# Kernel optimization log

Hardware: AMD Instinct MI355X
Metric: run time of the kernel (lower is better)

## Reference

```python
import jax, jax.numpy as jnp
import numpy as np
import math

EPS = 1e-5
H = 8  # n_heads


def _layernorm(x, g, b):
    mu = jnp.mean(x, axis=-1, keepdims=True)
    var = jnp.var(x, axis=-1, keepdims=True)
    return (x - mu) * jax.lax.rsqrt(var + EPS) * g + b


def _conv1d(x_bdn, w_oik):
    # x: [B, D, N], w: [O, I, K] (torch Conv1d layout), padding = K//2
    k = w_oik.shape[-1]
    p = k // 2
    return jax.lax.conv_general_dilated(
        x_bdn, w_oik, window_strides=(1,), padding=((p, p),),
        dimension_numbers=('NCH', 'OIH', 'NCH'))


def setup_inputs() -> dict:
    key = jax.random.key(0)
    ks = jax.random.split(key, 10)
    B, N, D, dq = 4096, 25, 256, 64
    s = 0.02
    inp = {
        'x': jax.random.normal(ks[0], (B, N, D), jnp.float32),
        'wq': jax.random.normal(ks[1], (D, D, 3), jnp.float32) * s,
        'wk': jax.random.normal(ks[2], (D, D, 3), jnp.float32) * s,
        'wv': jax.random.normal(ks[3], (D, D, 3), jnp.float32) * s,
        'ln_q_g': jnp.ones((D,), jnp.float32), 'ln_q_b': jnp.zeros((D,), jnp.float32),
        'ln_k_g': jnp.ones((D,), jnp.float32), 'ln_k_b': jnp.zeros((D,), jnp.float32),
        'ln_v_g': jnp.ones((D,), jnp.float32), 'ln_v_b': jnp.zeros((D,), jnp.float32),
        'rel_table': jax.random.normal(ks[4], (2 * N - 1, H), jnp.float32) * s,
        'global_bias': jax.random.normal(ks[5], (H, N, N), jnp.float32) * s,
        'alpha': jnp.float32(1.0),
        'wqf': jax.random.normal(ks[6], (D, dq), jnp.float32) * s,
        'bqf': jnp.zeros((dq,), jnp.float32),
        'wqp': jax.random.normal(ks[7], (dq, H), jnp.float32) * s,
        'bqp': jnp.zeros((H,), jnp.float32),
        'wo': jax.random.normal(ks[8], (D, D), jnp.float32) * s,
        'bo': jnp.zeros((D,), jnp.float32),
    }
    return inp


def reference(x, wq, wk, wv, ln_q_g, ln_q_b, ln_k_g, ln_k_b, ln_v_g, ln_v_b,
              rel_table, global_bias, alpha, wqf, bqf, wqp, bqp, wo, bo):
    B, N, D = x.shape
    dk = D // H
    xp = jnp.transpose(x, (0, 2, 1))  # [B, D, N]

    # conv projections + LayerNorm + residual
    q = x + _layernorm(jnp.transpose(_conv1d(xp, wq), (0, 2, 1)), ln_q_g, ln_q_b)
    k = x + _layernorm(jnp.transpose(_conv1d(xp, wk), (0, 2, 1)), ln_k_g, ln_k_b)
    v = x + _layernorm(jnp.transpose(_conv1d(xp, wv), (0, 2, 1)), ln_v_g, ln_v_b)

    q4 = q.reshape(B, N, H, dk)
    k4 = k.reshape(B, N, H, dk)
    v4 = v.reshape(B, N, H, dk)

    scores = jnp.einsum('bnhd,bmhd->bhnm', q4, k4) / math.sqrt(dk)

    # relative position bias: table[(i - j) + N - 1] -> [H, N, N]
    ids = jnp.arange(N)
    rel_idx = ids[:, None] - ids[None, :] + N - 1  # [N, N]
    rel_bias = jnp.transpose(rel_table[rel_idx], (2, 0, 1))  # [H, N, N]
    scores = scores + rel_bias[None] + global_bias[None] * alpha

    # dynamic adjacency bias from pairwise node feature differences
    qf = x @ wqf + bqf  # [B, N, dq]
    pair = jnp.tanh(qf[:, :, None, :] - qf[:, None, :, :])  # [B, N, N, dq]
    dyn = pair @ wqp + bqp  # [B, N, N, H]
    scores = scores + jnp.transpose(dyn, (0, 3, 1, 2))

    attn = jax.nn.softmax(scores, axis=-1)  # [B, H, N, N]
    out = jnp.einsum('bhnm,bmhd->bnhd', attn, v4).reshape(B, N, D)
    return out @ wo + bo
```

## Files before the change

### kernel.cpp

```cpp
#include <hip/hip_runtime.h>
#include <hip/hip_bf16.h>
#include <stdint.h>

using u16 = unsigned short;
using u32 = unsigned int;

typedef __attribute__((ext_vector_type(8))) __bf16 bf16x8;
typedef __attribute__((ext_vector_type(4))) float f32x4;

__device__ __forceinline__ float bf2f(u16 h) {
  u32 u = ((u32)h) << 16;
  return __builtin_bit_cast(float, u);
}
__device__ __forceinline__ u16 f2bf(float f) {
  u32 u = __builtin_bit_cast(u32, f);
  u += 0x7fffu + ((u >> 16) & 1u);
  return (u16)(u >> 16);
}
__device__ __forceinline__ float blo(u32 u) { return __builtin_bit_cast(float, u << 16); }
__device__ __forceinline__ float bhi(u32 u) { return __builtin_bit_cast(float, u & 0xffff0000u); }

__device__ __forceinline__ uint4 cvt8(const float* s) {
  float4 f0 = *(const float4*)s;
  float4 f1 = *(const float4*)(s + 4);
  uint4 r;
  r.x = (u32)f2bf(f0.x) | ((u32)f2bf(f0.y) << 16);
  r.y = (u32)f2bf(f0.z) | ((u32)f2bf(f0.w) << 16);
  r.z = (u32)f2bf(f1.x) | ((u32)f2bf(f1.y) << 16);
  r.w = (u32)f2bf(f1.z) | ((u32)f2bf(f1.w) << 16);
  return r;
}

__device__ __forceinline__ u32 tanh2(u32 a, u32 b) {
  const float d0 = blo(a) - blo(b);
  const float d1 = bhi(a) - bhi(b);
  const float e0 = __expf(2.f * d0), e1 = __expf(2.f * d1);
  const float t0 = 1.f - 2.f * __builtin_amdgcn_rcpf(e0 + 1.f);
  const float t1 = 1.f - 2.f * __builtin_amdgcn_rcpf(e1 + 1.f);
  return (u32)f2bf(t0) | ((u32)f2bf(t1) << 16);
}

__device__ __forceinline__ void gl_lds(const u16* gsrc, u16* ldsbase) {
  __builtin_amdgcn_global_load_lds(
      (const __attribute__((address_space(1))) u32*)gsrc,
      (__attribute__((address_space(3))) u32*)ldsbase, 16, 0, 0);
}


__global__ __launch_bounds__(256) void prep_kernel(
    const float* __restrict__ wq, const float* __restrict__ wk, const float* __restrict__ wv,
    const float* __restrict__ wo, const float* __restrict__ wqf,
    const float* __restrict__ lnqg, const float* __restrict__ lnqb,
    const float* __restrict__ lnkg, const float* __restrict__ lnkb,
    const float* __restrict__ lnvg, const float* __restrict__ lnvb,
    const float* __restrict__ relt, const float* __restrict__ gbias,
    const float* __restrict__ alphap,
    const float* __restrict__ wqp, const float* __restrict__ bqp,
    const float* __restrict__ bqf, const float* __restrict__ bo,
    u16* __restrict__ wT, u16* __restrict__ woT,
    u16* __restrict__ wqfT, u16* __restrict__ params)
{
  long long j = (long long)blockIdx.x * 256 + threadIdx.x;
  if (j < 589824) {
    int col = (int)(j / 768), k = (int)(j % 768);
    int p = col >> 8, o = col & 255, t = k >> 8, i = k & 255;
    const float* w = (p == 0) ? wq : (p == 1) ? wk : wv;
    wT[j] = f2bf(w[o * 768 + i * 3 + t]);
    return;
  }
  j -= 589824;
  if (j < 65536) {
    int n = (int)(j >> 8), k = (int)(j & 255);
    woT[j] = f2bf(wo[k * 256 + n]);
    return;
  }
  j -= 65536;
  if (j < 16384) {
    int col = (int)(j >> 8), k = (int)(j & 255);
    wqfT[j] = f2bf(wqf[k * 64 + col]);
    return;
  }
  j -= 16384;
  if (j < 8864) {
    int t = (int)j;
    if (t >= 8800) { params[t] = 0; return; }
    if (t >= 7776) {
      int t2 = t - 7776;
      int col = t2 >> 6, k = t2 & 63;
      params[t] = (col < 8) ? f2bf(wqp[k * 8 + col]) : (u16)0;
      return;
    }
    if (t >= 1928 && t < 6928) {
      int idx = t - 1928;
      int h = idx / 625, rem = idx % 625, n = rem / 25, m = rem % 25;
      params[t] = f2bf(gbias[idx] * alphap[0] + relt[(n - m + 24) * 8 + h] + bqp[h]);
      return;
    }
    const float* src; int si;
    if (t < 1536) {
      int a = t >> 8, c = t & 255;
      src = (a == 0) ? lnqg : (a == 1) ? lnqb : (a == 2) ? lnkg
          : (a == 3) ? lnkb : (a == 4) ? lnvg : lnvb;
      si = c;
    } else if (t < 1928) { src = relt;  si = t - 1536; }
    else if (t < 6936)   { src = alphap; si = 0; }
    else if (t < 7448)   { src = wqp;   si = t - 6936; }
    else if (t < 7456)   { src = bqp;   si = t - 7448; }
    else if (t < 7520)   { src = bqf;   si = t - 7456; }
    else                 { src = bo;    si = t - 7520; }
    params[t] = f2bf(src[si]);
  }
}

__global__ __launch_bounds__(256) void xconv_kernel(
    const float* __restrict__ x, u16* __restrict__ xbf)
{
  const long long i = ((long long)blockIdx.x * 256 + threadIdx.x) * 8;
  *(uint4*)&xbf[i] = cvt8(x + i);
}

__global__ __launch_bounds__(256) void convln_kernel(
    const u16* __restrict__ xbf, long long row0,
    const u16* __restrict__ wT,
    u16* __restrict__ C,
    const u16* __restrict__ params,
    const u16* __restrict__ zpad)
{
  __shared__ __align__(16) u16 Asm[64 * 64];
  __shared__ __align__(16) u16 Bsm[256 * 64];
  __shared__ float sG[256];
  __shared__ float sB[256];
  __shared__ float sSum[4][64];
  __shared__ float sSq[4][64];

  const int tid = threadIdx.x;
  const int l = tid & 63, w = tid >> 6;
  const int p = blockIdx.x;
  const int c0 = p * 256;
  const int r0 = blockIdx.y * 64;
  const int lrow = l >> 3, chunk = l & 7;
  const int g8 = (l >> 4) * 8, l15 = l & 15;
  const int rbase = 4 * (l >> 4);
  const int swz = l15 & 7;

  sG[tid] = bf2f(params[p * 512 + tid]);
  sB[tid] = bf2f(params[p * 512 + 256 + tid]);

  f32x4 acc[4][4];
#pragma unroll
  for (int m = 0; m < 4; ++m)
#pragma unroll
    for (int n = 0; n < 4; ++n)
      acc[m][n] = (f32x4){0.f, 0.f, 0.f, 0.f};

  for (int ks = 0; ks < 12; ++ks) {
    const int k0 = ks * 64;
    const int t = k0 >> 8, kc = k0 & 255;
    __syncthreads();
#pragma unroll
    for (int it = 0; it < 2; ++it) {
      const int seg = w * 2 + it;
      const int row_l = seg * 8 + lrow;
      const bool valid = ((unsigned)((r0 + row_l) % 25 + t - 1) < 25u);
      const u16* src = valid
          ? xbf + (size_t)(row0 + r0 + row_l + t - 1) * 256 + kc + ((chunk ^ lrow) << 3)
          : zpad;
      gl_lds(src, &Asm[seg * 512]);
    }
#pragma unroll
    for (int it = 0; it < 8; ++it) {
      const int seg = w * 8 + it;
      const int row_l = seg * 8 + lrow;
      const u16* src = wT + (size_t)(c0 + row_l) * 768 + k0 + ((chunk ^ lrow) << 3);
      gl_lds(src, &Bsm[seg * 512]);
    }
    __syncthreads();

#pragma unroll
    for (int kk = 0; kk < 64; kk += 32) {
      const int c = (kk >> 3) + (l >> 4);
      const int co = ((c ^ swz) << 3);
      bf16x8 av[4], bv[4];
#pragma unroll
      for (int m = 0; m < 4; ++m)
        av[m] = *(const bf16x8*)&Asm[(m * 16 + l15) * 64 + co];
#pragma unroll
      for (int n = 0; n < 4; ++n)
        bv[n] = *(const bf16x8*)&Bsm[(w * 64 + n * 16 + l15) * 64 + co];
#pragma unroll
      for (int m = 0; m < 4; ++m)
#pragma unroll
        for (int n = 0; n < 4; ++n)
          acc[m][n] = __builtin_amdgcn_mfma_f32_16x16x32_bf16(av[m], bv[n], acc[m][n], 0, 0, 0);
    }
  }

#pragma unroll
  for (int m = 0; m < 4; ++m) {
#pragma unroll
    for (int r = 0; r < 4; ++r) {
      float s = 0.f, q = 0.f;
#pragma unroll
      for (int n = 0; n < 4; ++n) { const float v = acc[m][n][r]; s += v; q += v * v; }
#pragma unroll
      for (int mk = 1; mk < 16; mk <<= 1) {
        s += __shfl_xor(s, mk, 64);
        q += __shfl_xor(q, mk, 64);
      }
      if (l15 == 0) {
        const int row = m * 16 + rbase + r;
        sSum[w][row] = s;
        sSq[w][row] = q;
      }
    }
  }
  __syncthreads();

#pragma unroll
  for (int m = 0; m < 4; ++m) {
    float mu4[4], rs4[4];
#pragma unroll
    for (int r = 0; r < 4; ++r) {
      const int row = m * 16 + rbase + r;
      const float tot = sSum[0][row] + sSum[1][row] + sSum[2][row] + sSum[3][row];
      const float tq  = sSq[0][row] + sSq[1][row] + sSq[2][row] + sSq[3][row];
      const float mu = tot * (1.f / 256.f);
      const float var = tq * (1.f / 256.f) - mu * mu;
      mu4[r] = mu;
      rs4[r] = rsqrtf(var + 1e-5f);
    }
#pragma unroll
    for (int n = 0; n < 4; ++n) {
      const int lc = w * 64 + n * 16 + l15;
      const float g = sG[lc], bb = sB[lc];
#pragma unroll
      for (int r = 0; r < 4; ++r) {
        const int row = m * 16 + rbase + r;
        const float xv = bf2f(xbf[(size_t)(row0 + r0 + row) * 256 + lc]);
        const float v = (acc[m][n][r] - mu4[r]) * rs4[r] * g + bb + xv;
        C[(size_t)(r0 + row) * 768 + c0 + lc] = f2bf(v);
      }
    }
  }
}

template<int BN, bool HAS_BIAS, bool F32OUT>
__global__ __launch_bounds__(256) void gemm_kernel(
    const u16* __restrict__ A, int lda, long long row0,
    const u16* __restrict__ BT, int ldb,
    void* __restrict__ Cv, int ldc,
    const u16* __restrict__ bias,
    int ksteps)
{
  constexpr int NB = BN / 32;
  __shared__ __align__(16) u16 Asm[128 * 64];
  __shared__ __align__(16) u16 Bsm[BN * 64];

  const int tid = threadIdx.x;
  const int l = tid & 63;
  const int w = tid >> 6;
  const int c0 = blockIdx.x * BN;
  const int r0 = blockIdx.y * 128;
  const int wr = w >> 1, wc = w & 1;

  f32x4 acc[4][NB];
#pragma unroll
  for (int m = 0; m < 4; ++m)
#pragma unroll
    for (int n = 0; n < NB; ++n)
      acc[m][n] = (f32x4){0.f, 0.f, 0.f, 0.f};

  const int lrow = l >> 3;
  const int chunk = l & 7;
  const int l15 = l & 15;
  const int swz = l15 & 7;

  for (int ks = 0; ks < ksteps; ++ks) {
    const int k0 = ks * 64;
    __syncthreads();
#pragma unroll
    for (int it = 0; it < 4; ++it) {
      const int seg = w * 4 + it;
      const int row_l = seg * 8 + lrow;
      const u16* src = A + (size_t)(row0 + r0 + row_l) * lda + k0 + ((chunk ^ lrow) << 3);
      gl_lds(src, &Asm[seg * 512]);
    }
#pragma unroll
    for (int it = 0; it < NB; ++it) {
      const int seg = w * NB + it;
      const int row_l = seg * 8 + lrow;
      const u16* src = BT + (size_t)(c0 + row_l) * ldb + k0 + ((chunk ^ lrow) << 3);
      gl_lds(src, &Bsm[seg * 512]);
    }
    __syncthreads();

#pragma unroll
    for (int kk = 0; kk < 64; kk += 32) {
      const int c = (kk >> 3) + (l >> 4);
      const int co = ((c ^ swz) << 3);
      bf16x8 av[4], bv[NB];
#pragma unroll
      for (int m = 0; m < 4; ++m)
        av[m] = *(const bf16x8*)&Asm[(wr * 64 + m * 16 + l15) * 64 + co];
#pragma unroll
      for (int n = 0; n < NB; ++n)
        bv[n] = *(const bf16x8*)&Bsm[(wc * (BN / 2) + n * 16 + l15) * 64 + co];
#pragma unroll
      for (int m = 0; m < 4; ++m)
#pragma unroll
        for (int n = 0; n < NB; ++n)
          acc[m][n] = __builtin_amdgcn_mfma_f32_16x16x32_bf16(av[m], bv[n], acc[m][n], 0, 0, 0);
    }
  }

  const int rbase = 4 * (l >> 4);
#pragma unroll
  for (int m = 0; m < 4; ++m) {
#pragma unroll
    for (int n = 0; n < NB; ++n) {
      const int col = c0 + wc * (BN / 2) + n * 16 + l15;
      float badd = 0.f;
      if (HAS_BIAS) badd = bf2f(bias[col]);
#pragma unroll
      for (int r = 0; r < 4; ++r) {
        const int row = r0 + wr * 64 + m * 16 + rbase + r;
        const float v = acc[m][n][r] + badd;
        if constexpr (F32OUT) ((float*)Cv)[(size_t)row * ldc + col] = v;
        else                  ((u16*)Cv)[(size_t)row * ldc + col] = f2bf(v);
      }
    }
  }
}

__global__ __launch_bounds__(256) void attn_kernel(
    u16* __restrict__ qkv,
    const u16* __restrict__ qf,
    const u16* __restrict__ params)
{
  __shared__ __align__(16) char arena[38848];
  float* sS    = (float*)arena;
  u16*   sV    = (u16*)(arena + 20000);
  u16*   sQF   = (u16*)(arena + 33200);
  u16*   sWQPT = (u16*)(arena + 36800);

  const int b = blockIdx.x;
  const int tid = threadIdx.x;
  const int w = tid >> 6, l = tid & 63;
  const int g8 = (l >> 4) * 8;
  const int rbase = 4 * (l >> 4);
  const int l15 = l & 15;

  {
    for (int i = tid; i < 800; i += 256) {
      const int m = i >> 5, c8 = (i & 31) * 8;
      *(uint4*)&sV[m * 264 + c8] =
          *(const uint4*)(qkv + (size_t)(b * 25 + m) * 768 + 512 + c8);
    }
    for (int i = tid; i < 200; i += 256) {
      const int r = i >> 3, c8 = (i & 7) * 8;
      *(uint4*)&sQF[r * 72 + c8] = *(const uint4*)(qf + (size_t)b * 1600 + r * 64 + c8);
    }
    for (int i = tid; i < 128; i += 256)
      ((uint4*)sWQPT)[i] = ((const uint4*)(params + 7776))[i];
  }
  __syncthreads();

  f32x4 dt[10];
  {
    const bf16x8 bv0 = *(const bf16x8*)&sWQPT[l15 * 64 + g8];
    const bf16x8 bv1 = *(const bf16x8*)&sWQPT[l15 * 64 + 32 + g8];
#pragma unroll
    for (int ti = 0; ti < 10; ++ti) {
      const int p0 = (ti * 4 + w) * 16;
      int p = p0 + l15; if (p > 624) p = 624;
      const int n = p / 25, m = p % 25;
      const uint4 qn0 = *(const uint4*)&sQF[n * 72 + g8];
      const uint4 qn1 = *(const uint4*)&sQF[n * 72 + 32 + g8];
      const uint4 qm0 = *(const uint4*)&sQF[m * 72 + g8];
      const uint4 qm1 = *(const uint4*)&sQF[m * 72 + 32 + g8];
      u32 a0[4], a1[4];
      a0[0] = tanh2(qn0.x, qm0.x); a0[1] = tanh2(qn0.y, qm0.y);
      a0[2] = tanh2(qn0.z, qm0.z); a0[3] = tanh2(qn0.w, qm0.w);
      a1[0] = tanh2(qn1.x, qm1.x); a1[1] = tanh2(qn1.y, qm1.y);
      a1[2] = tanh2(qn1.z, qm1.z); a1[3] = tanh2(qn1.w, qm1.w);
      const bf16x8 av0 = __builtin_bit_cast(bf16x8, *(uint4*)a0);
      const bf16x8 av1 = __builtin_bit_cast(bf16x8, *(uint4*)a1);
      f32x4 d = (f32x4){0.f, 0.f, 0.f, 0.f};
      d = __builtin_amdgcn_mfma_f32_16x16x32_bf16(av0, bv0, d, 0, 0, 0);
      d = __builtin_amdgcn_mfma_f32_16x16x32_bf16(av1, bv1, d, 0, 0, 0);
      dt[ti] = d;
    }
    bf16x8 zf8;
#pragma unroll
    for (int j = 0; j < 8; ++j) zf8[j] = (__bf16)0.f;
#pragma unroll
    for (int hh = 0; hh < 2; ++hh) {
      const int h = 2 * w + hh;
      bf16x8 qa[2], kb[2];
#pragma unroll
      for (int t = 0; t < 2; ++t) {
        const int row = l15 + 16 * t;
        if (row < 25) {
          const u16* base = qkv + (size_t)(b * 25 + row) * 768 + h * 32 + g8;
          qa[t] = *(const bf16x8*)base;
          kb[t] = *(const bf16x8*)(base + 256);
        } else { qa[t] = zf8; kb[t] = zf8; }
      }
#pragma unroll
      for (int tn = 0; tn < 2; ++tn)
#pragma unroll
        for (int tm = 0; tm < 2; ++tm) {
          f32x4 d = __builtin_amdgcn_mfma_f32_16x16x32_bf16(
              qa[tn], kb[tm], (f32x4){0.f, 0.f, 0.f, 0.f}, 0, 0, 0);
          const int m = l15 + 16 * tm;
#pragma unroll
          for (int r = 0; r < 4; ++r) {
            const int n = rbase + r + 16 * tn;
            if (n < 25 && m < 25) {
              const int idx = h * 625 + n * 25 + m;
              sS[idx] = d[r] * 0.17677669529663687f + bf2f(params[1928 + idx]);
            }
          }
        }
    }
  }
  __syncthreads();

  {
    if (l15 < 8) {
      const int h = l15;
#pragma unroll
      for (int ti = 0; ti < 10; ++ti) {
        const int p0 = (ti * 4 + w) * 16;
#pragma unroll
        for (int r = 0; r < 4; ++r) {
          const int p = p0 + rbase + r;
          if (p < 625) sS[h * 625 + p] += dt[ti][r];
        }
      }
    }
  }
  __syncthreads();

  {
    for (int u = tid; u < 200; u += 256) {
      const int h = u / 25, n = u % 25;
      float* rp = &sS[h * 625 + n * 25];
      float mx = -1e30f;
#pragma unroll
      for (int m = 0; m < 25; ++m) mx = fmaxf(mx, rp[m]);
      float ssum = 0.f;
#pragma unroll
      for (int m = 0; m < 25; ++m) { rp[m] = __expf(rp[m] - mx); ssum += rp[m]; }
      const float inv = __builtin_amdgcn_rcpf(ssum);
#pragma unroll
      for (int m = 0; m < 25; ++m) rp[m] *= inv;
    }
  }
  __syncthreads();

  {
#pragma unroll
    for (int hh = 0; hh < 2; ++hh) {
      const int h = 2 * w + hh;
      bf16x8 pa[2], vb[2];
#pragma unroll
      for (int t = 0; t < 2; ++t) {
        const int n = l15 + 16 * t;
#pragma unroll
        for (int j = 0; j < 8; ++j) {
          const int m = g8 + j;
          const float pv = (n < 25 && m < 25) ? sS[h * 625 + n * 25 + m] : 0.f;
          pa[t][j] = (__bf16)pv;
        }
      }
#pragma unroll
      for (int t = 0; t < 2; ++t) {
        const int dcol = l15 + 16 * t;
#pragma unroll
        for (int j = 0; j < 8; ++j) {
          const int m = g8 + j;
          vb[t][j] = (m < 25)
              ? __builtin_bit_cast(__bf16, sV[m * 264 + h * 32 + dcol])
              : (__bf16)0.f;
        }
      }
#pragma unroll
      for (int tn = 0; tn < 2; ++tn)
#pragma unroll
        for (int td = 0; td < 2; ++td) {
          f32x4 d = __builtin_amdgcn_mfma_f32_16x16x32_bf16(
              pa[tn], vb[td], (f32x4){0.f, 0.f, 0.f, 0.f}, 0, 0, 0);
          const int dcol = l15 + 16 * td;
#pragma unroll
          for (int r = 0; r < 4; ++r) {
            const int n = rbase + r + 16 * tn;
            if (n < 25)
              qkv[(size_t)(b * 25 + n) * 768 + h * 32 + dcol] = f2bf(d[r]);
          }
        }
    }
  }
}

extern "C" void kernel_launch(void* const* d_in, const int* in_sizes, int n_in,
                              void* d_out, int out_size, void* d_ws, size_t ws_size,
                              hipStream_t stream) {
  (void)in_sizes; (void)n_in; (void)out_size;
  const float* x    = (const float*)d_in[0];
  const float* wq   = (const float*)d_in[1];
  const float* wk   = (const float*)d_in[2];
  const float* wv   = (const float*)d_in[3];
  const float* lnqg = (const float*)d_in[4];
  const float* lnqb = (const float*)d_in[5];
  const float* lnkg = (const float*)d_in[6];
  const float* lnkb = (const float*)d_in[7];
  const float* lnvg = (const float*)d_in[8];
  const float* lnvb = (const float*)d_in[9];
  const float* relt = (const float*)d_in[10];
  const float* gbias= (const float*)d_in[11];
  const float* alph = (const float*)d_in[12];
  const float* wqf  = (const float*)d_in[13];
  const float* bqf  = (const float*)d_in[14];
  const float* wqp  = (const float*)d_in[15];
  const float* bqp  = (const float*)d_in[16];
  const float* wo   = (const float*)d_in[17];
  const float* bo   = (const float*)d_in[18];

  char* ws = (char*)d_ws;
  u16* params = (u16*)(ws + 0);
  u16* wT     = (u16*)(ws + 32768);
  u16* woT    = (u16*)(ws + 1212416);
  u16* wqfT   = (u16*)(ws + 1343488);
  const size_t fixed_bytes = 1376256;
  const size_t xbf_bytes = 52428800;
  const size_t per_batch = 41600;
  u16* zpad = params + 8800;

  int CB = 4096;
  while (CB > 128 && fixed_bytes + xbf_bytes + (size_t)CB * per_batch > ws_size) CB >>= 1;
  const int nchunks = 4096 / CB;
  const int rows = CB * 25;

  u16* x_bf = (u16*)(ws + fixed_bytes);
  const size_t chunk_off = fixed_bytes + xbf_bytes;
  u16* qkv_c = (u16*)(ws + chunk_off);
  u16* qf_c  = (u16*)(ws + chunk_off + (size_t)CB * 38400);
  float* outf = (float*)d_out;

  prep_kernel<<<2659, 256, 0, stream>>>(
      wq, wk, wv, wo, wqf, lnqg, lnqb, lnkg, lnkb, lnvg, lnvb,
      relt, gbias, alph, wqp, bqp, bqf, bo,
      wT, woT, wqfT, params);
  xconv_kernel<<<12800, 256, 0, stream>>>(x, x_bf);

  for (int c = 0; c < nchunks; ++c) {
    const long long R0 = (long long)c * rows;

    convln_kernel<<<dim3(3, rows / 64), 256, 0, stream>>>(
        x_bf, R0, wT, qkv_c, params, zpad);

    gemm_kernel<64, true, false><<<dim3(1, rows / 128), 256, 0, stream>>>(
        x_bf, 256, R0, wqfT, 256, qf_c, 64, params + 7456, 4);

    attn_kernel<<<CB, 256, 0, stream>>>(qkv_c, qf_c, params);

    gemm_kernel<128, true, true><<<dim3(2, rows / 128), 256, 0, stream>>>(
        qkv_c, 768, 0, woT, 256, outf + (size_t)R0 * 256, 256, params + 7520, 4);
  }
}
```

Baseline: 382.6 us.

## Fuse qf projection GEMM into conv-LN kernel and enlarge row tile to 128

The conv+LayerNorm kernel now runs 512 threads over 128-row tiles with a 2x4 wave grid, and a fourth blockIdx.x slice computes the x@wqf+bqf projection, so the separate qf gemm launch is removed. Fewer launches and more A-tile reuse per weight tile are the intended savings. The qf blocks do far less work than the conv blocks, which can leave the grid load-imbalanced, and the larger block with 16 accumulators per thread may lower occupancy.

Result: slower. 415.4 us (+8.6%).

```diff
diff --git a/kernel.cpp b/kernel.cpp
--- a/kernel.cpp
+++ b/kernel.cpp
@@ -119,126 +119,174 @@
   *(uint4*)&xbf[i] = cvt8(x + i);
 }
 
-__global__ __launch_bounds__(256) void convln_kernel(
+__global__ __launch_bounds__(512) void convln_kernel(
     const u16* __restrict__ xbf, long long row0,
-    const u16* __restrict__ wT,
+    const u16* __restrict__ wT, const u16* __restrict__ wqfT,
     u16* __restrict__ C,
+    u16* __restrict__ qfc,
     const u16* __restrict__ params,
     const u16* __restrict__ zpad)
 {
-  __shared__ __align__(16) u16 Asm[64 * 64];
+  __shared__ __align__(16) u16 Asm[128 * 64];
   __shared__ __align__(16) u16 Bsm[256 * 64];
   __shared__ float sG[256];
   __shared__ float sB[256];
-  __shared__ float sSum[4][64];
-  __shared__ float sSq[4][64];
+  __shared__ float sSum[4][128];
+  __shared__ float sSq[4][128];
 
   const int tid = threadIdx.x;
   const int l = tid & 63, w = tid >> 6;
   const int p = blockIdx.x;
-  const int c0 = p * 256;
-  const int r0 = blockIdx.y * 64;
+  const int r0 = blockIdx.y * 128;
   const int lrow = l >> 3, chunk = l & 7;
   const int g8 = (l >> 4) * 8, l15 = l & 15;
   const int rbase = 4 * (l >> 4);
   const int swz = l15 & 7;
 
-  sG[tid] = bf2f(params[p * 512 + tid]);
-  sB[tid] = bf2f(params[p * 512 + 256 + tid]);
-
-  f32x4 acc[4][4];
-#pragma unroll
-  for (int m = 0; m < 4; ++m)
-#pragma unroll
-    for (int n = 0; n < 4; ++n)
-      acc[m][n] = (f32x4){0.f, 0.f, 0.f, 0.f};
-
-  for (int ks = 0; ks < 12; ++ks) {
-    const int k0 = ks * 64;
-    const int t = k0 >> 8, kc = k0 & 255;
+  if (p < 3) {
+    const int c0 = p * 256;
+    if (tid < 256) sG[tid] = bf2f(params[p * 512 + tid]);
+    else           sB[tid - 256] = bf2f(params[p * 512 + 256 + (tid - 256)]);
+    const int wr = w >> 2, wc = w & 3;
+
+    f32x4 acc[4][4];
+#pragma unroll
+    for (int m = 0; m < 4; ++m)
+#pragma unroll
+      for (int n = 0; n < 4; ++n)
+        acc[m][n] = (f32x4){0.f, 0.f, 0.f, 0.f};
+
+    for (int ks = 0; ks < 12; ++ks) {
+      const int k0 = ks * 64;
+      const int t = k0 >> 8, kc = k0 & 255;
+      __syncthreads();
+#pragma unroll
+      for (int it = 0; it < 2; ++it) {
+        const int seg = w * 2 + it;
+        const int row_l = seg * 8 + lrow;
+        const bool valid = ((unsigned)((r0 + row_l) % 25 + t - 1) < 25u);
+        const u16* src = valid
+            ? xbf + (size_t)(row0 + r0 + row_l + t - 1) * 256 + kc + ((chunk ^ lrow) << 3)
+            : zpad;
+        gl_lds(src, &Asm[seg * 512]);
+      }
+#pragma unroll
+      for (int it = 0; it < 4; ++it) {
+        const int seg = w * 4 + it;
+        const int row_l = seg * 8 + lrow;
+        const u16* src = wT + (size_t)(c0 + row_l) * 768 + k0 + ((chunk ^ lrow) << 3);
+        gl_lds(src, &Bsm[seg * 512]);
+      }
+      __syncthreads();
+
+#pragma unroll
+      for (int kk = 0; kk < 64; kk += 32) {
+        const int c = (kk >> 3) + (l >> 4);
+        const int co = ((c ^ swz) << 3);
+        bf16x8 av[4], bv[4];
+#pragma unroll
+        for (int m = 0; m < 4; ++m)
+          av[m] = *(const bf16x8*)&Asm[(wr * 64 + m * 16 + l15) * 64 + co];
+#pragma unroll
+        for (int n = 0; n < 4; ++n)
+          bv[n] = *(const bf16x8*)&Bsm[(wc * 64 + n * 16 + l15) * 64 + co];
+#pragma unroll
+        for (int m = 0; m < 4; ++m)
+#pragma unroll
+          for (int n = 0; n < 4; ++n)
+            acc[m][n] = __builtin_amdgcn_mfma_f32_16x16x32_bf16(av[m], bv[n], acc[m][n], 0, 0, 0);
+      }
+    }
+
+#pragma unroll
+    for (int m = 0; m < 4; ++m) {
+#pragma unroll
+      for (int r = 0; r < 4; ++r) {
+        float s = 0.f, q = 0.f;
+#pragma unroll
+        for (int n = 0; n < 4; ++n) { const float v = acc[m][n][r]; s += v; q += v * v; }
+#pragma unroll
+        for (int mk = 1; mk < 16; mk <<= 1) {
+          s += __shfl_xor(s, mk, 64);
+          q += __shfl_xor(q, mk, 64);
+        }
+        if (l15 == 0) {
+          const int row = wr * 64 + m * 16 + rbase + r;
+          sSum[wc][row] = s;
+          sSq[wc][row] = q;
+        }
+      }
+    }
     __syncthreads();
-#pragma unroll
-    for (int it = 0; it < 2; ++it) {
-      const int seg = w * 2 + it;
-      const int row_l = seg * 8 + lrow;
-      const bool valid = ((unsigned)((r0 + row_l) % 25 + t - 1) < 25u);
-      const u16* src = valid
-          ? xbf + (size_t)(row0 + r0 + row_l + t - 1) * 256 + kc + ((chunk ^ lrow) << 3)
-          : zpad;
-      gl_lds(src, &Asm[seg * 512]);
-    }
-#pragma unroll
-    for (int it = 0; it < 8; ++it) {
-      const int seg = w * 8 + it;
-      const int row_l = seg * 8 + lrow;
-      const u16* src = wT + (size_t)(c0 + row_l) * 768 + k0 + ((chunk ^ lrow) << 3);
-      gl_lds(src, &Bsm[seg * 512]);
-    }
-    __syncthreads();
-
-#pragma unroll
-    for (int kk = 0; kk < 64; kk += 32) {
-      const int c = (kk >> 3) + (l >> 4);
-      const int co = ((c ^ swz) << 3);
-      bf16x8 av[4], bv[4];
-#pragma unroll
-      for (int m = 0; m < 4; ++m)
-        av[m] = *(const bf16x8*)&Asm[(m * 16 + l15) * 64 + co];
-#pragma unroll
-      for (int n = 0; n < 4; ++n)
-        bv[n] = *(const bf16x8*)&Bsm[(w * 64 + n * 16 + l15) * 64 + co];
-#pragma unroll
-      for (int m = 0; m < 4; ++m)
-#pragma unroll
-        for (int n = 0; n < 4; ++n)
-          acc[m][n] = __builtin_amdgcn_mfma_f32_16x16x32_bf16(av[m], bv[n], acc[m][n], 0, 0, 0);
-    }
-  }
-
-#pragma unroll
-  for (int m = 0; m < 4; ++m) {
-#pragma unroll
-    for (int r = 0; r < 4; ++r) {
-      float s = 0.f, q = 0.f;
-#pragma unroll
-      for (int n = 0; n < 4; ++n) { const float v = acc[m][n][r]; s += v; q += v * v; }
-#pragma unroll
-      for (int mk = 1; mk < 16; mk <<= 1) {
-        s += __shfl_xor(s, mk, 64);
-        q += __shfl_xor(q, mk, 64);
-      }
-      if (l15 == 0) {
-        const int row = m * 16 + rbase + r;
-        sSum[w][row] = s;
-        sSq[w][row] = q;
-      }
-    }
-  }
-  __syncthreads();
-
-#pragma unroll
-  for (int m = 0; m < 4; ++m) {
-    float mu4[4], rs4[4];
-#pragma unroll
-    for (int r = 0; r < 4; ++r) {
-      const int row = m * 16 + rbase + r;
-      const float tot = sSum[0][row] + sSum[1][row] + sSum[2][row] + sSum[3][row];
-      const float tq  = sSq[0][row] + sSq[1][row] + sSq[2][row] + sSq[3][row];
-      const float mu = tot * (1.f / 256.f);
-      const float var = tq * (1.f / 256.f) - mu * mu;
-      mu4[r] = mu;
-      rs4[r] = rsqrtf(var + 1e-5f);
+
+#pragma unroll
+    for (int m = 0; m < 4; ++m) {
+      float mu4[4], rs4[4];
+#pragma unroll
+      for (int r = 0; r < 4; ++r) {
+        const int row = wr * 64 + m * 16 + rbase + r;
+        const float tot = sSum[0][row] + sSum[1][row] + sSum[2][row] + sSum[3][row];
+        const float tq  = sSq[0][row] + sSq[1][row] + sSq[2][row] + sSq[3][row];
+        const float mu = tot * (1.f / 256.f);
+        const float var = tq * (1.f / 256.f) - mu * mu;
+        mu4[r] = mu;
+        rs4[r] = rsqrtf(var + 1e-5f);
+      }
+#pragma unroll
+      for (int n = 0; n < 4; ++n) {
+        const int lc = wc * 64 + n * 16 + l15;
+        const float g = sG[lc], bb = sB[lc];
+#pragma unroll
+        for (int r = 0; r < 4; ++r) {
+          const int row = wr * 64 + m * 16 + rbase + r;
+          const float xv = bf2f(xbf[(size_t)(row0 + r0 + row) * 256 + lc]);
+          const float v = (acc[m][n][r] - mu4[r]) * rs4[r] * g + bb + xv;
+          C[(size_t)(r0 + row) * 768 + c0 + lc] = f2bf(v);
+        }
+      }
+    }
+  } else {
+    f32x4 acc2[4];
+#pragma unroll
+    for (int n = 0; n < 4; ++n) acc2[n] = (f32x4){0.f, 0.f, 0.f, 0.f};
+
+    for (int ks2 = 0; ks2 < 4; ++ks2) {
+      __syncthreads();
+#pragma unroll
+      for (int it = 0; it < 2; ++it) {
+        const int seg = w * 2 + it;
+        const int row_l = seg * 8 + lrow;
+        const u16* src = xbf + (size_t)(row0 + r0 + row_l) * 256 + ks2 * 64
+                       + ((chunk ^ lrow) << 3);
+        gl_lds(src, &Asm[seg * 512]);
+      }
+      {
+        const int row_l = w * 8 + lrow;
+        const u16* src = wqfT + (size_t)row_l * 256 + ks2 * 64 + ((chunk ^ lrow) << 3);
+        gl_lds(src, &Bsm[w * 512]);
+      }
+      __syncthreads();
+
+#pragma unroll
+      for (int kk = 0; kk < 64; kk += 32) {
+        const int c = (kk >> 3) + (l >> 4);
+        const int co = ((c ^ swz) << 3);
+        const bf16x8 av = *(const bf16x8*)&Asm[(w * 16 + l15) * 64 + co];
+#pragma unroll
+        for (int n = 0; n < 4; ++n) {
+          const bf16x8 bv = *(const bf16x8*)&Bsm[(n * 16 + l15) * 64 + co];
+          acc2[n] = __builtin_amdgcn_mfma_f32_16x16x32_bf16(av, bv, acc2[n], 0, 0, 0);
+        }
+      }
     }
 #pragma unroll
     for (int n = 0; n < 4; ++n) {
-      const int lc = w * 64 + n * 16 + l15;
-      const float g = sG[lc], bb = sB[lc];
+      const int col = n * 16 + l15;
+      const float badd = bf2f(params[7456 + col]);
 #pragma unroll
       for (int r = 0; r < 4; ++r) {
-        const int row = m * 16 + rbase + r;
-        const float xv = bf2f(xbf[(size_t)(row0 + r0 + row) * 256 + lc]);
-        const float v = (acc[m][n][r] - mu4[r]) * rs4[r] * g + bb + xv;
-        C[(size_t)(r0 + row) * 768 + c0 + lc] = f2bf(v);
+        const int row = r0 + w * 16 + rbase + r;
+        qfc[(size_t)row * 64 + col] = f2bf(acc2[n][r] + badd);
       }
     }
   }
@@ -557,11 +605,8 @@
   for (int c = 0; c < nchunks; ++c) {
     const long long R0 = (long long)c * rows;
 
-    convln_kernel<<<dim3(3, rows / 64), 256, 0, stream>>>(
-        x_bf, R0, wT, qkv_c, params, zpad);
-
-    gemm_kernel<64, true, false><<<dim3(1, rows / 128), 256, 0, stream>>>(
-        x_bf, 256, R0, wqfT, 256, qf_c, 64, params + 7456, 4);
+    convln_kernel<<<dim3(4, rows / 128), 512, 0, stream>>>(
+        x_bf, R0, wT, wqfT, qkv_c, qf_c, params, zpad);
 
     attn_kernel<<<CB, 256, 0, stream>>>(qkv_c, qf_c, params);
 
```
